# Optimization experiments

Measured on AMD Instinct MI355X. Metric: run time of the kernel, lower is better.

The kernel has to match this reference:

```python
import jax, jax.numpy as jnp
import numpy as np
from jax import lax

N, H, BS = 256, 1024, 128
ALPHA, BETA, SIGMA = 60.0, 20.0, 5.0
EPS = 1e-8


def _mlp_w(key, n_in, n_out):
    return jax.random.normal(key, (n_out, n_in), dtype=jnp.float32) / np.sqrt(n_in)


def setup_inputs() -> dict:
    key = jax.random.key(0)
    ks = jax.random.split(key, 8)
    inp = {
        "t": jnp.zeros((), dtype=jnp.float32),
        "x": jax.random.normal(ks[0], (BS, N), dtype=jnp.float32),
        "Wf1": _mlp_w(ks[1], N, H), "bf1": jnp.zeros((H,), jnp.float32),
        "Wf2": _mlp_w(ks[2], H, N), "bf2": jnp.zeros((N,), jnp.float32),
        "Wg1": _mlp_w(ks[3], N, H), "bg1": jnp.zeros((H,), jnp.float32),
        "Wg2": _mlp_w(ks[4], H, N), "bg2": jnp.zeros((N,), jnp.float32),
        "Wk1": _mlp_w(ks[5], N, H), "bk1": jnp.zeros((H,), jnp.float32),
        "Wk2": _mlp_w(ks[6], H, N), "bk2": jnp.zeros((N,), jnp.float32),
    }
    return inp


def reference(t, x, Wf1, bf1, Wf2, bf2, Wg1, bg1, Wg2, bg2, Wk1, bk1, Wk2, bk2):
    def mlp(u, W1, b1, W2, b2):
        return jnp.tanh(u @ W1.T + b1) @ W2.T + b2

    def k_func(u):
        return mlp(u, Wk1, bk1, Wk2, bk2)

    f_out = mlp(x, Wf1, bf1, Wf2, bf2)          # f_model(t, x); t unused
    k_out = k_func(x)
    G_k_out = mlp(x, Wg1, bg1, Wg2, bg2)        # g_fn(x)[0]
    dx_dt = f_out + G_k_out

    # compute_k_jacobian: torch detaches u, so no grad flows to x here.
    # torch layout: J[b, j, i] = d k_i / d u_j  (transpose of jacfwd output)
    x_d = lax.stop_gradient(x)
    J_fwd = jax.vmap(jax.jacfwd(k_func))(x_d)   # [bs, i_out, j_in]
    J_x = jnp.swapaxes(J_fwd, 1, 2)             # [bs, j, i]

    k_norm = jnp.linalg.norm(k_out, axis=1)                      # [bs]
    Jf = jnp.einsum('bji,bi->bj', J_x, f_out)                    # bmm(J, f)
    Jf_norm = jnp.linalg.norm(Jf, axis=1)
    c1 = Jf_norm - ALPHA * k_norm ** (2 * SIGMA - 1)
    JG = jnp.einsum('bji,bi->bj', J_x, G_k_out)                  # bmm(J, G)
    c2 = jnp.sum(k_out * JG, axis=1) - BETA * k_norm ** (2 * SIGMA)

    mask = (c1 > EPS) | (c2 < -EPS)                              # [bs]
    dx_upd = jnp.where(mask[:, None], jnp.zeros_like(dx_dt), dx_dt)
    return (dx_upd + dx_dt) / 2
```

## Files before the change

### kernel.cpp

```cpp
#include <hip/hip_runtime.h>
#include <stdint.h>

#define N_ 256
#define H_ 1024
#define BS_ 128

#define WS_SK    0
#define WS_OACC  131072
#define WS_OPART 229376
#define WS_JPART 3375104
#define WS_FLOATS 4423680

__global__ __launch_bounds__(256) void k12s(
    const float* __restrict__ x,
    const float* __restrict__ Wf1, const float* __restrict__ bf1,
    const float* __restrict__ Wg1, const float* __restrict__ bg1,
    const float* __restrict__ Wk1, const float* __restrict__ bk1,
    const float* __restrict__ Wf2, const float* __restrict__ bf2,
    const float* __restrict__ Wg2, const float* __restrict__ bg2,
    const float* __restrict__ Wk2, const float* __restrict__ bk2,
    float* __restrict__ sk, float* __restrict__ opart)
{
    const int bx  = blockIdx.x;
    const int sid = (bx & 7) * 96 + (bx >> 3);
    const int g   = sid >> 3;
    const int rt  = sid & 7;
    const int m   = g >> 5;
    const int ht  = g & 31;
    const int t   = threadIdx.x;
    const int h0  = ht * 32;
    const int r0  = rt * 16;

    const float* W1 = (m == 0) ? Wf1 : (m == 1) ? Wg1 : Wk1;
    const float* b1 = (m == 0) ? bf1 : (m == 1) ? bg1 : bk1;
    const float* W2 = (m == 0) ? Wf2 : (m == 1) ? Wg2 : Wk2;
    const float* b2 = (m == 0) ? bf2 : (m == 1) ? bg2 : bk2;

    __shared__ float4 wbuf[2048];
    __shared__ __align__(16) float xs[16][256];
    __shared__ __align__(16) float ts[16][32];

    {
        const float4* xsrc = (const float4*)(x + r0 * N_);
        #pragma unroll
        for (int v = 0; v < 4; ++v)
            ((float4*)xs)[t + 256 * v] = xsrc[t + 256 * v];
        const float4* wg = (const float4*)(W1 + h0 * N_);
        #pragma unroll
        for (int v = 0; v < 8; ++v) {
            const int f4  = t + 256 * v;
            const int row = f4 >> 6, c = f4 & 63;
            wbuf[(row << 6) | (c & 48) | ((c & 15) ^ (row & 15))] = wg[f4];
        }
    }
    __syncthreads();

    {
        const int hl   = t & 15;
        const int kq   = (t >> 4) & 3;
        const int hgrp = (t >> 6) & 1;
        const int rh   = t >> 7;
        const int hloc = hgrp * 16 + hl;
        const int h    = h0 + hloc;

        float acc[8] = {0.f,0.f,0.f,0.f,0.f,0.f,0.f,0.f};
        const float4* wrow = wbuf + (hloc << 6) + (kq << 4);
        #pragma unroll
        for (int cl = 0; cl < 16; ++cl) {
            const float4 wv = wrow[cl ^ hl];
            #pragma unroll
            for (int r = 0; r < 8; ++r) {
                const float4 xv = ((const float4*)xs[rh * 8 + r])[(kq << 4) + cl];
                acc[r] += wv.x*xv.x + wv.y*xv.y + wv.z*xv.z + wv.w*xv.w;
            }
        }
        #pragma unroll
        for (int r = 0; r < 8; ++r) {
            acc[r] += __shfl_xor(acc[r], 16, 64);
            acc[r] += __shfl_xor(acc[r], 32, 64);
        }
        float va = acc[0], vb = acc[1];
        va = (kq == 1) ? acc[2] : va;  vb = (kq == 1) ? acc[3] : vb;
        va = (kq == 2) ? acc[4] : va;  vb = (kq == 2) ? acc[5] : vb;
        va = (kq == 3) ? acc[6] : va;  vb = (kq == 3) ? acc[7] : vb;
        const float bv = b1[h];
        const float v0 = tanhf(va + bv), v1 = tanhf(vb + bv);
        const int rl = rh * 8 + kq * 2;
        ts[rl][hloc]     = v0;
        ts[rl + 1][hloc] = v1;
        if (m == 2) {
            sk[(r0 + rl) * H_ + h]     = 1.0f - v0 * v0;
            sk[(r0 + rl + 1) * H_ + h] = 1.0f - v1 * v1;
        }
    }
    __syncthreads();

    {
        #pragma unroll
        for (int v = 0; v < 8; ++v) {
            const int idx = t + 256 * v;
            const int row = idx >> 3, c = idx & 7;
            wbuf[(row << 3) | (c ^ (row & 7))] =
                ((const float4*)(W2 + row * H_ + h0))[c];
        }
    }
    __syncthreads();

    {
        float acc[16];
        const float bv2 = (ht == 0) ? b2[t] : 0.0f;
        #pragma unroll
        for (int r = 0; r < 16; ++r) acc[r] = bv2;

        const float4* wrow = wbuf + (t << 3);
        #pragma unroll
        for (int c = 0; c < 8; ++c) {
            const float4 wv = wrow[c ^ (t & 7)];
            #pragma unroll
            for (int r = 0; r < 16; ++r) {
                const float4 av = ((const float4*)ts[r])[c];
                acc[r] += wv.x*av.x + wv.y*av.y + wv.z*av.z + wv.w*av.w;
            }
        }
        #pragma unroll
        for (int r = 0; r < 16; ++r)
            opart[((ht * 3 + m) * BS_ + r0 + r) * N_ + t] = acc[r];
    }
}

__global__ __launch_bounds__(256) void k25_reduce(
    const float* __restrict__ opart, float* __restrict__ oacc)
{
    const int tid = blockIdx.x * 256 + threadIdx.x;
    float s = 0.f;
    #pragma unroll
    for (int ks = 0; ks < 32; ++ks)
        s += opart[ks * (3 * BS_ * N_) + tid];
    oacc[tid] = s;
}

__global__ __launch_bounds__(256) void k3_vj(
    const float* __restrict__ Wk1, const float* __restrict__ Wk2,
    const float* __restrict__ oacc, const float* __restrict__ sk,
    float* __restrict__ jpart)
{
    const int q  = blockIdx.x & 15;
    const int rp = blockIdx.x >> 4;
    const int t  = threadIdx.x;
    const int r0 = rp * 4;
    const int h0 = q * 64;

    __shared__ float fos[4][256], gos[4][256];
    __shared__ float sfv[4][64], sgv[4][64];

    for (int u = t; u < 1024; u += 256) {
        const int r = u >> 8, i = u & 255;
        fos[r][i] = oacc[(r0 + r) * N_ + i];
        gos[r][i] = oacc[(BS_ + r0 + r) * N_ + i];
    }
    __syncthreads();

    {
        const int hl = t & 63;
        const int rl = t >> 6;
        const int h  = h0 + hl;
        const float* w2 = Wk2 + h;
        float vf = 0.f, vg = 0.f;
        #pragma unroll 8
        for (int c = 0; c < 64; ++c) {
            const float4 of = ((const float4*)fos[rl])[c];
            const float4 og = ((const float4*)gos[rl])[c];
            const float w0  = w2[(4 * c + 0) * H_];
            const float w1v = w2[(4 * c + 1) * H_];
            const float w2v = w2[(4 * c + 2) * H_];
            const float w3  = w2[(4 * c + 3) * H_];
            vf += of.x * w0 + of.y * w1v + of.z * w2v + of.w * w3;
            vg += og.x * w0 + og.y * w1v + og.z * w2v + og.w * w3;
        }
        const float s = sk[(r0 + rl) * H_ + h];
        sfv[rl][hl] = s * vf;
        sgv[rl][hl] = s * vg;
    }
    __syncthreads();

    {
        float jf[4] = {0.f, 0.f, 0.f, 0.f};
        float jg[4] = {0.f, 0.f, 0.f, 0.f};
        const float* w1 = Wk1 + h0 * N_ + t;
        #pragma unroll 4
        for (int c = 0; c < 16; ++c) {
            const float w0  = w1[(4 * c + 0) * N_];
            const float wv1 = w1[(4 * c + 1) * N_];
            const float wv2 = w1[(4 * c + 2) * N_];
            const float wv3 = w1[(4 * c + 3) * N_];
            #pragma unroll
            for (int r = 0; r < 4; ++r) {
                const float4 sf = ((const float4*)sfv[r])[c];
                const float4 sg = ((const float4*)sgv[r])[c];
                jf[r] += sf.x * w0 + sf.y * wv1 + sf.z * wv2 + sf.w * wv3;
                jg[r] += sg.x * w0 + sg.y * wv1 + sg.z * wv2 + sg.w * wv3;
            }
        }
        #pragma unroll
        for (int r = 0; r < 4; ++r) {
            jpart[((q * 2 + 0) * BS_ + r0 + r) * N_ + t] = jf[r];
            jpart[((q * 2 + 1) * BS_ + r0 + r) * N_ + t] = jg[r];
        }
    }
}

__global__ __launch_bounds__(256) void k4_final(
    const float* __restrict__ oacc,
    const float* __restrict__ jpart,
    float* __restrict__ out)
{
    const int r = blockIdx.x;
    const int t = threadIdx.x;
    __shared__ float red[12];

    const float fo = oacc[r * N_ + t];
    const float go = oacc[(BS_ + r) * N_ + t];
    const float ko = oacc[(2 * BS_ + r) * N_ + t];

    float jf = 0.f, jg = 0.f;
    #pragma unroll
    for (int q = 0; q < 16; ++q) {
        jf += jpart[((q * 2 + 0) * BS_ + r) * N_ + t];
        jg += jpart[((q * 2 + 1) * BS_ + r) * N_ + t];
    }

    float v0 = ko * ko, v1 = jf * jf, v2 = ko * jg;
    #pragma unroll
    for (int o = 32; o > 0; o >>= 1) {
        v0 += __shfl_xor(v0, o, 64);
        v1 += __shfl_xor(v1, o, 64);
        v2 += __shfl_xor(v2, o, 64);
    }
    const int wid = t >> 6;
    if ((t & 63) == 0) {
        red[wid * 3 + 0] = v0;
        red[wid * 3 + 1] = v1;
        red[wid * 3 + 2] = v2;
    }
    __syncthreads();
    const float kn2 = red[0] + red[3] + red[6] + red[9];
    const float jf2 = red[1] + red[4] + red[7] + red[10];
    const float kjg = red[2] + red[5] + red[8] + red[11];

    const float knorm = sqrtf(kn2);
    const float kn4 = kn2 * kn2;
    const float kn8 = kn4 * kn4;
    const float c1 = sqrtf(jf2) - 60.0f * kn8 * knorm;
    const float c2 = kjg - 20.0f * kn8 * kn2;
    const float scale = ((c1 > 1e-8f) || (c2 < -1e-8f)) ? 0.5f : 1.0f;

    out[r * N_ + t] = (fo + go) * scale;
}

__global__ __launch_bounds__(256) void manifold_fused(
    const float* __restrict__ x,
    const float* __restrict__ Wf1, const float* __restrict__ bf1v,
    const float* __restrict__ Wf2, const float* __restrict__ bf2v,
    const float* __restrict__ Wg1, const float* __restrict__ bg1v,
    const float* __restrict__ Wg2, const float* __restrict__ bg2v,
    const float* __restrict__ Wk1, const float* __restrict__ bk1v,
    const float* __restrict__ Wk2, const float* __restrict__ bk2v,
    float* __restrict__ out)
{
    const int b = blockIdx.x;
    const int t = threadIdx.x;
    __shared__ float xs[N_];
    __shared__ float tf[H_], tg[H_], tk[H_], sk[H_];
    __shared__ float fo[N_], go[N_];
    __shared__ float sfv[H_], sgv[H_];
    __shared__ float red[12];

    xs[t] = x[b * N_ + t];
    __syncthreads();
    {
        float acc[12];
        const float4* rows[12];
        #pragma unroll
        for (int m = 0; m < 4; ++m) {
            const int h = t + m * 256;
            rows[m]     = (const float4*)(Wf1 + h * N_);
            rows[4 + m] = (const float4*)(Wg1 + h * N_);
            rows[8 + m] = (const float4*)(Wk1 + h * N_);
            acc[m] = bf1v[h]; acc[4 + m] = bg1v[h]; acc[8 + m] = bk1v[h];
        }
        const float4* xs4 = (const float4*)xs;
        #pragma unroll 2
        for (int c = 0; c < 64; ++c) {
            float4 a = xs4[c];
            #pragma unroll
            for (int r = 0; r < 12; ++r) {
                float4 w = rows[r][c];
                acc[r] += w.x * a.x + w.y * a.y + w.z * a.z + w.w * a.w;
            }
        }
        #pragma unroll
        for (int m = 0; m < 4; ++m) {
            const int h = t + m * 256;
            float vtf = tanhf(acc[m]);
            float vtg = tanhf(acc[4 + m]);
            float vtk = tanhf(acc[8 + m]);
            tf[h] = vtf; tg[h] = vtg; tk[h] = vtk; sk[h] = 1.0f - vtk * vtk;
        }
    }
    __syncthreads();
    float af = bf2v[t], ag = bg2v[t], ak = bk2v[t];
    {
        const float4* rf = (const float4*)(Wf2 + t * H_);
        const float4* rg = (const float4*)(Wg2 + t * H_);
        const float4* rk = (const float4*)(Wk2 + t * H_);
        #pragma unroll 2
        for (int c = 0; c < 256; ++c) {
            float4 wf = rf[c], wg = rg[c], wk = rk[c];
            float4 vf = ((const float4*)tf)[c];
            af += wf.x*vf.x + wf.y*vf.y + wf.z*vf.z + wf.w*vf.w;
            float4 vg = ((const float4*)tg)[c];
            ag += wg.x*vg.x + wg.y*vg.y + wg.z*vg.z + wg.w*vg.w;
            float4 vk = ((const float4*)tk)[c];
            ak += wk.x*vk.x + wk.y*vk.y + wk.z*vk.z + wk.w*vk.w;
        }
    }
    fo[t] = af; go[t] = ag;
    __syncthreads();
    {
        float vf[4] = {0.f,0.f,0.f,0.f}, vg[4] = {0.f,0.f,0.f,0.f};
        const float* base = Wk2 + 4 * t;
        #pragma unroll 4
        for (int i = 0; i < N_; ++i) {
            float4 w = *(const float4*)(base + i * H_);
            float fv = fo[i], gv = go[i];
            vf[0]+=w.x*fv; vf[1]+=w.y*fv; vf[2]+=w.z*fv; vf[3]+=w.w*fv;
            vg[0]+=w.x*gv; vg[1]+=w.y*gv; vg[2]+=w.z*gv; vg[3]+=w.w*gv;
        }
        #pragma unroll
        for (int c = 0; c < 4; ++c) {
            sfv[4*t+c] = sk[4*t+c]*vf[c];
            sgv[4*t+c] = sk[4*t+c]*vg[c];
        }
    }
    __syncthreads();
    float jf = 0.f, jg = 0.f;
    {
        const float* col = Wk1 + t;
        #pragma unroll 4
        for (int c = 0; c < 256; ++c) {
            float4 s4 = ((const float4*)sfv)[c];
            float4 g4 = ((const float4*)sgv)[c];
            const int h = c * 4;
            float w0 = col[(h+0)*N_], w1 = col[(h+1)*N_];
            float w2 = col[(h+2)*N_], w3 = col[(h+3)*N_];
            jf += s4.x*w0 + s4.y*w1 + s4.z*w2 + s4.w*w3;
            jg += g4.x*w0 + g4.y*w1 + g4.z*w2 + g4.w*w3;
        }
    }
    float v0 = ak*ak, v1 = jf*jf, v2 = ak*jg;
    #pragma unroll
    for (int o = 32; o > 0; o >>= 1) {
        v0 += __shfl_xor(v0, o, 64);
        v1 += __shfl_xor(v1, o, 64);
        v2 += __shfl_xor(v2, o, 64);
    }
    const int wid = t >> 6;
    if ((t & 63) == 0) {
        red[wid*3+0] = v0; red[wid*3+1] = v1; red[wid*3+2] = v2;
    }
    __syncthreads();
    const float kn2 = red[0]+red[3]+red[6]+red[9];
    const float jf2 = red[1]+red[4]+red[7]+red[10];
    const float kjg = red[2]+red[5]+red[8]+red[11];
    const float knorm = sqrtf(kn2);
    const float kn4 = kn2*kn2, kn8 = kn4*kn4;
    const float c1 = sqrtf(jf2) - 60.0f*kn8*knorm;
    const float c2 = kjg - 20.0f*kn8*kn2;
    const float scale = ((c1 > 1e-8f) || (c2 < -1e-8f)) ? 0.5f : 1.0f;
    out[b*N_+t] = (af+ag)*scale;
}

extern "C" void kernel_launch(void* const* d_in, const int* in_sizes, int n_in,
                              void* d_out, int out_size, void* d_ws, size_t ws_size,
                              hipStream_t stream) {
    const float* x    = (const float*)d_in[1];
    const float* Wf1  = (const float*)d_in[2];
    const float* bf1v = (const float*)d_in[3];
    const float* Wf2  = (const float*)d_in[4];
    const float* bf2v = (const float*)d_in[5];
    const float* Wg1  = (const float*)d_in[6];
    const float* bg1v = (const float*)d_in[7];
    const float* Wg2  = (const float*)d_in[8];
    const float* bg2v = (const float*)d_in[9];
    const float* Wk1  = (const float*)d_in[10];
    const float* bk1v = (const float*)d_in[11];
    const float* Wk2  = (const float*)d_in[12];
    const float* bk2v = (const float*)d_in[13];
    float* out = (float*)d_out;

    if (ws_size < (size_t)WS_FLOATS * sizeof(float)) {
        manifold_fused<<<BS_, 256, 0, stream>>>(
            x, Wf1, bf1v, Wf2, bf2v, Wg1, bg1v, Wg2, bg2v,
            Wk1, bk1v, Wk2, bk2v, out);
        return;
    }

    float* ws    = (float*)d_ws;
    float* sk    = ws + WS_SK;
    float* oacc  = ws + WS_OACC;
    float* opart = ws + WS_OPART;
    float* jpart = ws + WS_JPART;

    k12s      <<<768, 256, 0, stream>>>(x, Wf1, bf1v, Wg1, bg1v, Wk1, bk1v,
                                        Wf2, bf2v, Wg2, bg2v, Wk2, bk2v,
                                        sk, opart);
    k25_reduce<<<384, 256, 0, stream>>>(opart, oacc);
    k3_vj     <<<512, 256, 0, stream>>>(Wk1, Wk2, oacc, sk, jpart);
    k4_final  <<<BS_, 256, 0, stream>>>(oacc, jpart, out);
}
```

Measured before the change: 121.2 us.

## Re-tile first MLP kernel with 4x4 register blocking and padded LDS

Restructures both GEMM stages of the fused first-layer/second-layer kernel so that each thread computes a 4-hidden-unit by 4-row register tile instead of one hidden unit over 8 or 16 rows. This increases register-level reuse of weight and activation loads from LDS. It also changes the LDS swizzles and pads the x and tanh buffers to avoid bank conflicts, and it vectorises the opart stores as float4. The cost is one extra shuffle stage in the reduction and more complex index selection.

```diff
diff --git a/kernel.cpp b/kernel.cpp
--- a/kernel.cpp
+++ b/kernel.cpp
@@ -11,7 +11,11 @@
 #define WS_JPART 3375104
 #define WS_FLOATS 4423680
 
-__global__ __launch_bounds__(256) void k12s(
+__device__ __forceinline__ float dot4(float4 a, float4 b) {
+    return a.x * b.x + a.y * b.y + a.z * b.z + a.w * b.w;
+}
+
+__global__ __launch_bounds__(256) void k12t(
     const float* __restrict__ x,
     const float* __restrict__ Wf1, const float* __restrict__ bf1,
     const float* __restrict__ Wg1, const float* __restrict__ bg1,
@@ -37,55 +41,76 @@
     const float* b2 = (m == 0) ? bf2 : (m == 1) ? bg2 : bk2;
 
     __shared__ float4 wbuf[2048];
-    __shared__ __align__(16) float xs[16][256];
-    __shared__ __align__(16) float ts[16][32];
+    __shared__ __align__(16) float xs[16][260];
+    __shared__ __align__(16) float ts[16][36];
 
     {
         const float4* xsrc = (const float4*)(x + r0 * N_);
         #pragma unroll
-        for (int v = 0; v < 4; ++v)
-            ((float4*)xs)[t + 256 * v] = xsrc[t + 256 * v];
+        for (int v = 0; v < 4; ++v) {
+            const int u = t + 256 * v;
+            const int row = u >> 6, i = u & 63;
+            ((float4*)(xs[row]))[i] = xsrc[u];
+        }
         const float4* wg = (const float4*)(W1 + h0 * N_);
         #pragma unroll
         for (int v = 0; v < 8; ++v) {
-            const int f4  = t + 256 * v;
-            const int row = f4 >> 6, c = f4 & 63;
-            wbuf[(row << 6) | (c & 48) | ((c & 15) ^ (row & 15))] = wg[f4];
-        }
-    }
-    __syncthreads();
-
-    {
-        const int hl   = t & 15;
-        const int kq   = (t >> 4) & 3;
-        const int hgrp = (t >> 6) & 1;
-        const int rh   = t >> 7;
-        const int hloc = hgrp * 16 + hl;
+            const int u = t + 256 * v;
+            const int row = u >> 6, c = u & 63;
+            wbuf[(row << 6) | (c ^ (row & 7))] = wg[u];
+        }
+    }
+    __syncthreads();
+
+    {
+        const int hl = t & 7;
+        const int ke = (t >> 3) & 7;
+        const int rq = t >> 6;
+        const int x4b = (hl & 1) << 2;
+
+        float acc[4][4];
+        #pragma unroll
+        for (int a = 0; a < 4; ++a)
+            #pragma unroll
+            for (int b = 0; b < 4; ++b) acc[a][b] = 0.f;
+
+        const float4* wbase = wbuf + ((hl * 4) << 6);
+        #pragma unroll
+        for (int c = 0; c < 8; ++c) {
+            const int kap = c * 8 + ke;
+            const float4 w0 = wbase[0 * 64 + (kap ^ x4b ^ 0)];
+            const float4 w1 = wbase[1 * 64 + (kap ^ x4b ^ 1)];
+            const float4 w2v = wbase[2 * 64 + (kap ^ x4b ^ 2)];
+            const float4 w3 = wbase[3 * 64 + (kap ^ x4b ^ 3)];
+            #pragma unroll
+            for (int rr = 0; rr < 4; ++rr) {
+                const float4 xv =
+                    *(const float4*)(xs[rq * 4 + rr] + kap * 4);
+                acc[0][rr] += dot4(w0, xv);
+                acc[1][rr] += dot4(w1, xv);
+                acc[2][rr] += dot4(w2v, xv);
+                acc[3][rr] += dot4(w3, xv);
+            }
+        }
+        #pragma unroll
+        for (int a = 0; a < 4; ++a)
+            #pragma unroll
+            for (int b = 0; b < 4; ++b) {
+                acc[a][b] += __shfl_xor(acc[a][b], 8, 64);
+                acc[a][b] += __shfl_xor(acc[a][b], 16, 64);
+                acc[a][b] += __shfl_xor(acc[a][b], 32, 64);
+            }
+        const int hh = ke >> 1;
+        const int rb = (ke & 1) * 2;
+        float o0 = acc[0][rb],     o1 = acc[0][rb + 1];
+        o0 = (hh == 1) ? acc[1][rb] : o0;  o1 = (hh == 1) ? acc[1][rb + 1] : o1;
+        o0 = (hh == 2) ? acc[2][rb] : o0;  o1 = (hh == 2) ? acc[2][rb + 1] : o1;
+        o0 = (hh == 3) ? acc[3][rb] : o0;  o1 = (hh == 3) ? acc[3][rb + 1] : o1;
+        const int hloc = hl * 4 + hh;
         const int h    = h0 + hloc;
-
-        float acc[8] = {0.f,0.f,0.f,0.f,0.f,0.f,0.f,0.f};
-        const float4* wrow = wbuf + (hloc << 6) + (kq << 4);
-        #pragma unroll
-        for (int cl = 0; cl < 16; ++cl) {
-            const float4 wv = wrow[cl ^ hl];
-            #pragma unroll
-            for (int r = 0; r < 8; ++r) {
-                const float4 xv = ((const float4*)xs[rh * 8 + r])[(kq << 4) + cl];
-                acc[r] += wv.x*xv.x + wv.y*xv.y + wv.z*xv.z + wv.w*xv.w;
-            }
-        }
-        #pragma unroll
-        for (int r = 0; r < 8; ++r) {
-            acc[r] += __shfl_xor(acc[r], 16, 64);
-            acc[r] += __shfl_xor(acc[r], 32, 64);
-        }
-        float va = acc[0], vb = acc[1];
-        va = (kq == 1) ? acc[2] : va;  vb = (kq == 1) ? acc[3] : vb;
-        va = (kq == 2) ? acc[4] : va;  vb = (kq == 2) ? acc[5] : vb;
-        va = (kq == 3) ? acc[6] : va;  vb = (kq == 3) ? acc[7] : vb;
         const float bv = b1[h];
-        const float v0 = tanhf(va + bv), v1 = tanhf(vb + bv);
-        const int rl = rh * 8 + kq * 2;
+        const float v0 = tanhf(o0 + bv), v1 = tanhf(o1 + bv);
+        const int rl = rq * 4 + rb;
         ts[rl][hloc]     = v0;
         ts[rl + 1][hloc] = v1;
         if (m == 2) {
@@ -98,33 +123,53 @@
     {
         #pragma unroll
         for (int v = 0; v < 8; ++v) {
-            const int idx = t + 256 * v;
-            const int row = idx >> 3, c = idx & 7;
-            wbuf[(row << 3) | (c ^ (row & 7))] =
+            const int u = t + 256 * v;
+            const int row = u >> 3, c = u & 7;
+            wbuf[(row << 3) | (c ^ ((row >> 2) & 7))] =
                 ((const float4*)(W2 + row * H_ + h0))[c];
         }
     }
     __syncthreads();
 
     {
-        float acc[16];
-        const float bv2 = (ht == 0) ? b2[t] : 0.0f;
-        #pragma unroll
-        for (int r = 0; r < 16; ++r) acc[r] = bv2;
-
-        const float4* wrow = wbuf + (t << 3);
+        const int is = t & 63;
+        const int rq = t >> 6;
+        const int sw = is & 7;
+
+        float4 acc[4];
+        #pragma unroll
+        for (int rr = 0; rr < 4; ++rr) acc[rr] = make_float4(0.f, 0.f, 0.f, 0.f);
+
+        const float4* w2b = wbuf + ((is * 4) << 3);
         #pragma unroll
         for (int c = 0; c < 8; ++c) {
-            const float4 wv = wrow[c ^ (t & 7)];
-            #pragma unroll
-            for (int r = 0; r < 16; ++r) {
-                const float4 av = ((const float4*)ts[r])[c];
-                acc[r] += wv.x*av.x + wv.y*av.y + wv.z*av.z + wv.w*av.w;
-            }
-        }
-        #pragma unroll
-        for (int r = 0; r < 16; ++r)
-            opart[((ht * 3 + m) * BS_ + r0 + r) * N_ + t] = acc[r];
+            const float4 wv0 = w2b[0 * 8 + (c ^ sw)];
+            const float4 wv1 = w2b[1 * 8 + (c ^ sw)];
+            const float4 wv2 = w2b[2 * 8 + (c ^ sw)];
+            const float4 wv3 = w2b[3 * 8 + (c ^ sw)];
+            #pragma unroll
+            for (int rr = 0; rr < 4; ++rr) {
+                const float4 av = *(const float4*)(ts[rq * 4 + rr] + c * 4);
+                acc[rr].x += dot4(wv0, av);
+                acc[rr].y += dot4(wv1, av);
+                acc[rr].z += dot4(wv2, av);
+                acc[rr].w += dot4(wv3, av);
+            }
+        }
+        if (ht == 0) {
+            const int i = is * 4;
+            const float4 bv = make_float4(b2[i], b2[i + 1], b2[i + 2], b2[i + 3]);
+            #pragma unroll
+            for (int rr = 0; rr < 4; ++rr) {
+                acc[rr].x += bv.x; acc[rr].y += bv.y;
+                acc[rr].z += bv.z; acc[rr].w += bv.w;
+            }
+        }
+        #pragma unroll
+        for (int rr = 0; rr < 4; ++rr) {
+            const int r = r0 + rq * 4 + rr;
+            ((float4*)(opart + ((ht * 3 + m) * BS_ + r) * N_))[is] = acc[rr];
+        }
     }
 }
 
@@ -411,7 +456,7 @@
     float* opart = ws + WS_OPART;
     float* jpart = ws + WS_JPART;
 
-    k12s      <<<768, 256, 0, stream>>>(x, Wf1, bf1v, Wg1, bg1v, Wk1, bk1v,
+    k12t      <<<768, 256, 0, stream>>>(x, Wf1, bf1v, Wg1, bg1v, Wk1, bk1v,
                                         Wf2, bf2v, Wg2, bg2v, Wk2, bk2v,
                                         sk, opart);
     k25_reduce<<<384, 256, 0, stream>>>(opart, oacc);
```

Measured after the change: 124.6 us. 1.03x slower.
